# Kernel optimization log

Hardware: AMD Instinct MI355X
Metric: run time of the kernel (lower is better)

## Reference

```python
import jax, jax.numpy as jnp
import numpy as np

# Block(type='a'): dim=256, mlp_ratio=2, qk_dim=64, att_cr=0.5 (pdim=128), sr=2, inp_group=1
DIM, QK, PD, HID, SR = 256, 64, 128, 512, 2
EPS = 1e-5
SCALE = QK ** -0.5


def _conv(x, w, stride=1, pad=0, groups=1):
    return jax.lax.conv_general_dilated(
        x, w, (stride, stride), [(pad, pad), (pad, pad)],
        feature_group_count=groups,
        dimension_numbers=('NCHW', 'OIHW', 'NCHW'))


def _bn(x, s, b):
    # BatchNorm2d in inference/reparam form: per-channel affine
    return x * s[:, None, None] + b[:, None, None]


def setup_inputs() -> dict:
    key = jax.random.key(0)
    ks = jax.random.split(key, 16)
    B, H, W = 16, 64, 64
    x = jax.random.normal(ks[0], (B, DIM, H, W), jnp.float32)
    def w(k, shape):  # conv weights
        return jax.random.normal(k, shape, jnp.float32) * 0.02
    def sb(k, c):     # bn scale / bias
        k1, k2 = jax.random.split(k)
        return (1.0 + 0.1 * jax.random.normal(k1, (c,), jnp.float32),
                0.1 * jax.random.normal(k2, (c,), jnp.float32))
    s_in, b_in = sb(ks[2], 2 * QK + DIM)
    s_k, b_k = sb(ks[4], QK)
    s_v, b_v = sb(ks[6], PD)
    s_out, b_out = sb(ks[8], DIM)
    s1, b1 = sb(ks[10], HID)
    s2, b2 = sb(ks[12], DIM)
    return dict(
        x=x,
        gn_w=1.0 + 0.1 * jax.random.normal(ks[13], (DIM,), jnp.float32),
        gn_b=0.1 * jax.random.normal(ks[14], (DIM,), jnp.float32),
        w_in=w(ks[1], (2 * QK + DIM, DIM, 3, 3)), s_in=s_in, b_in=b_in,
        w_k=w(ks[3], (QK, 1, SR, SR)), s_k=s_k, b_k=b_k,
        w_v=w(ks[5], (PD, 1, SR, SR)), s_v=s_v, b_v=b_v,
        w_out=w(ks[7], (DIM, DIM, 1, 1)), s_out=s_out, b_out=b_out,
        w1=w(ks[9], (HID, DIM, 1, 1)), s1=s1, b1=b1,
        w2=w(ks[11], (DIM, HID, 1, 1)), s2=s2, b2=b2,
    )


def reference(x, gn_w, gn_b, w_in, s_in, b_in, w_k, s_k, b_k, w_v, s_v, b_v,
              w_out, s_out, b_out, w1, s1, b1, w2, s2, b2):
    B, _, H, W = x.shape
    # --- LRSHA branch ---
    # GroupNorm(1, dim): normalize over (C,H,W) per sample, per-channel affine
    mu = jnp.mean(x, axis=(1, 2, 3), keepdims=True)
    var = jnp.var(x, axis=(1, 2, 3), keepdims=True)
    xn = (x - mu) * jax.lax.rsqrt(var + EPS)
    xn = xn * gn_w[:, None, None] + gn_b[:, None, None]
    t = _bn(_conv(xn, w_in, stride=1, pad=1), s_in, b_in)  # [B, 2*QK+DIM, H, W]
    q, k, v, u = jnp.split(t, [QK, 2 * QK, 2 * QK + PD], axis=1)
    k = _bn(_conv(k, w_k, stride=SR, groups=QK), s_k, b_k)  # [B,QK,H/2,W/2]
    v = _bn(_conv(v, w_v, stride=SR, groups=PD), s_v, b_v)  # [B,PD,H/2,W/2]
    qf = q.reshape(B, QK, H * W)          # [B, QK, N]
    kf = k.reshape(B, QK, -1)             # [B, QK, M]
    vf = v.reshape(B, PD, -1)             # [B, PD, M]
    attn = jax.nn.softmax(jnp.einsum('bcn,bcm->bnm', qf, kf) * SCALE, axis=-1)
    a = jnp.einsum('bpm,bnm->bpn', vf, attn).reshape(B, PD, H, W)
    cat = jnp.concatenate([a, u], axis=1)  # [B, DIM, H, W]
    att_out = _bn(_conv(jax.nn.relu(cat), w_out), s_out, b_out)
    x1 = x + att_out  # residual
    # --- FFN branch (1x1 conv -> ReLU -> 1x1 conv) ---
    h = jax.nn.relu(_bn(_conv(x1, w1), s1, b1))
    ffn = _bn(_conv(h, w2), s2, b2)
    return x1 + ffn
```

## Files before the change

### kernel.cpp

```cpp
#include <hip/hip_runtime.h>
#include <hip/hip_bf16.h>

#define DIM 256
#define QK 64
#define PD 128
#define HID 512
#define NPX 4096
#define NB 16
#define SCALE 0.125f
#define GN_EPS 1e-5f

typedef short bf16x8 __attribute__((ext_vector_type(8)));
typedef float f32x4 __attribute__((ext_vector_type(4)));
#define MFMA16(a, b, c) __builtin_amdgcn_mfma_f32_16x16x32_bf16(a, b, c, 0, 0, 0)

__device__ __forceinline__ unsigned f2b(float f) {
    unsigned u = __float_as_uint(f);
    return (u + 0x7fffu + ((u >> 16) & 1u)) >> 16;
}
__device__ __forceinline__ float b2f(unsigned short s) {
    return __uint_as_float((unsigned)s << 16);
}

__global__ __launch_bounds__(256) void gn_part_kernel(const float* __restrict__ x, float* __restrict__ part) {
    int chunk = blockIdx.x, b = blockIdx.y;
    const float* xp = x + (size_t)b * (DIM * NPX) + (size_t)chunk * 16384;
    float s = 0.f, ss = 0.f;
    for (int i = threadIdx.x; i < 16384; i += 256) { float v = xp[i]; s += v; ss += v * v; }
    for (int off = 32; off > 0; off >>= 1) { s += __shfl_down(s, off); ss += __shfl_down(ss, off); }
    __shared__ float red[8];
    int w = threadIdx.x >> 6;
    if ((threadIdx.x & 63) == 0) { red[w * 2] = s; red[w * 2 + 1] = ss; }
    __syncthreads();
    if (threadIdx.x == 0) {
        float S = red[0] + red[2] + red[4] + red[6];
        float SS = red[1] + red[3] + red[5] + red[7];
        part[(b * 64 + chunk) * 2] = S;
        part[(b * 64 + chunk) * 2 + 1] = SS;
    }
}

__global__ __launch_bounds__(256) void gn_final_kernel(const float* __restrict__ part,
                                                       const float* __restrict__ gn_w, const float* __restrict__ gn_b,
                                                       float* __restrict__ Aarr, float* __restrict__ Barr) {
    int b = blockIdx.x;
    float s = 0.f, ss = 0.f;
    if (threadIdx.x < 64) {
        s = part[(b * 64 + threadIdx.x) * 2];
        ss = part[(b * 64 + threadIdx.x) * 2 + 1];
        for (int off = 32; off > 0; off >>= 1) { s += __shfl_down(s, off); ss += __shfl_down(ss, off); }
    }
    __shared__ float sh[2];
    if (threadIdx.x == 0) {
        const float invN = 1.f / (float)(DIM * NPX);
        float mu = s * invN;
        float var = ss * invN - mu * mu;
        sh[0] = mu; sh[1] = rsqrtf(var + GN_EPS);
    }
    __syncthreads();
    float mu = sh[0], rstd = sh[1];
    int c = threadIdx.x;
    float g = gn_w[c] * rstd;
    Aarr[b * 256 + c] = g;
    Barr[b * 256 + c] = gn_b[c] - mu * g;
}

__global__ __launch_bounds__(256) void xnb_kernel(const float* __restrict__ x,
                                                  const float* __restrict__ Aarr, const float* __restrict__ Barr,
                                                  unsigned short* __restrict__ xb) {
    int y = blockIdx.x, b = blockIdx.y;
    int tid = threadIdx.x;
    __shared__ unsigned short tile[64 * 264];
    const float* xr = x + ((size_t)b << 20) + (size_t)y * 64;
    const float* Ab = Aarr + b * 256;
    const float* Bb = Barr + b * 256;
    for (int it = 0; it < 64; it++) {
        int lin = it * 256 + tid;
        int c = lin >> 6, px = lin & 63;
        float v = fmaf(xr[((size_t)c << 12) + px], Ab[c], Bb[c]);
        tile[px * 264 + c] = (unsigned short)f2b(v);
    }
    __syncthreads();
    unsigned short* ob = xb + (((size_t)(b * 64 + y)) << 14);
    for (int it = 0; it < 8; it++) {
        int lin = it * 256 + tid;
        int px = lin >> 5, g = lin & 31;
        *(uint4*)&ob[px * 256 + g * 8] = *(const uint4*)&tile[px * 264 + g * 8];
    }
}

__global__ __launch_bounds__(256) void wcvt_kernel(const float* __restrict__ w_in, const float* __restrict__ w_out,
                                                   const float* __restrict__ w1, const float* __restrict__ w2,
                                                   unsigned short* __restrict__ wb2, unsigned short* __restrict__ wob,
                                                   unsigned short* __restrict__ w1b, unsigned short* __restrict__ w2b) {
    int idx = blockIdx.x * 256 + threadIdx.x;
    if (idx < 884736) {
        int ci = idx & 31;
        int oc = (idx >> 5) % 384;
        int tapck = idx / 12288;
        int ck = tapck / 9, tap = tapck % 9;
        wb2[idx] = (unsigned short)f2b(w_in[((size_t)oc * 256 + ck * 32 + ci) * 9 + tap]);
    } else if (idx < 950272) {
        int j = idx - 884736;
        wob[j] = (unsigned short)f2b(w_out[j]);
    } else if (idx < 1081344) {
        int j = idx - 950272;
        w1b[j] = (unsigned short)f2b(w1[j]);
    } else if (idx < 1212416) {
        int j = idx - 1081344;
        w2b[j] = (unsigned short)f2b(w2[j]);
    }
}

__global__ __launch_bounds__(256, 3) void conv3_mfma_kernel(const unsigned short* __restrict__ xb,
                                                            const unsigned short* __restrict__ wb2,
                                                            const float* __restrict__ s_in, const float* __restrict__ b_in,
                                                            unsigned short* __restrict__ tcl) {
    int wgid = blockIdx.x;
    int tile = (wgid & 7) * 96 + (wgid >> 3);
    int ocb = tile % 6;
    int tmp = tile / 6;
    int rg2 = tmp & 7, b = tmp >> 3;
    int tid = threadIdx.x;
    int w = tid >> 6, lane = tid & 63, g = lane >> 4, l15 = lane & 15;
    __shared__ unsigned short xs[6 * 66 * 40];
    int oc0 = ocb * 64;
    if (tid < 48) {
        int row = tid >> 3, cp = (tid >> 2) & 1, gg = tid & 3;
        int col = cp ? 65 : 0;
        *(uint4*)&xs[(row * 66 + col) * 40 + gg * 8] = make_uint4(0, 0, 0, 0);
    }
    const unsigned short* xg = xb + ((size_t)b << 20);
    for (int half = 0; half < 2; half++) {
        int y0 = rg2 * 8 + half * 4;
        f32x4 acc[4][4];
#pragma unroll
        for (int o = 0; o < 4; o++)
#pragma unroll
            for (int p = 0; p < 4; p++)
#pragma unroll
                for (int r = 0; r < 4; r++) acc[o][p][r] = 0.f;
        for (int ck = 0; ck < 8; ck++) {
            int ci0 = ck * 32;
            __syncthreads();
#pragma unroll
            for (int it = 0; it < 6; it++) {
                int lin = it * 256 + tid;
                int gg = lin & 3, col = (lin >> 2) & 63, row = lin >> 8;
                int y = y0 - 1 + row;
                uint4 val = make_uint4(0, 0, 0, 0);
                if (y >= 0 && y < 64)
                    val = *(const uint4*)(xg + (((size_t)(y * 64 + col)) << 8) + ci0 + gg * 8);
                *(uint4*)&xs[(row * 66 + col + 1) * 40 + gg * 8] = val;
            }
            __syncthreads();
            const unsigned short* wp = wb2 + (size_t)ck * 9 * 384 * 32;
#pragma unroll
            for (int tap = 0; tap < 9; tap++) {
                int dy = tap / 3, dx = tap % 3;
                bf16x8 Af[4], Bf[4];
#pragma unroll
                for (int o = 0; o < 4; o++)
                    Af[o] = *(const bf16x8*)(wp + ((size_t)tap * 384 + oc0 + o * 16 + l15) * 32 + g * 8);
#pragma unroll
                for (int p = 0; p < 4; p++)
                    Bf[p] = *(const bf16x8*)&xs[((w + dy) * 66 + p * 16 + l15 + dx) * 40 + g * 8];
#pragma unroll
                for (int o = 0; o < 4; o++)
#pragma unroll
                    for (int p = 0; p < 4; p++)
                        acc[o][p] = MFMA16(Af[o], Bf[p], acc[o][p]);
            }
        }
        int y = y0 + w;
        unsigned short* tout = tcl + ((size_t)(b * 4096 + y * 64)) * 384;
#pragma unroll
        for (int o = 0; o < 4; o++) {
            int ocb4 = oc0 + o * 16 + 4 * g;
            float s0 = s_in[ocb4], s1 = s_in[ocb4 + 1], s2 = s_in[ocb4 + 2], s3 = s_in[ocb4 + 3];
            float b0 = b_in[ocb4], b1 = b_in[ocb4 + 1], b2 = b_in[ocb4 + 2], b3 = b_in[ocb4 + 3];
#pragma unroll
            for (int p = 0; p < 4; p++) {
                ushort4 h;
                h.x = (unsigned short)f2b(fmaf(acc[o][p][0], s0, b0));
                h.y = (unsigned short)f2b(fmaf(acc[o][p][1], s1, b1));
                h.z = (unsigned short)f2b(fmaf(acc[o][p][2], s2, b2));
                h.w = (unsigned short)f2b(fmaf(acc[o][p][3], s3, b3));
                *(ushort4*)&tout[(size_t)(p * 16 + l15) * 384 + ocb4] = h;
            }
        }
    }
}

__global__ __launch_bounds__(256) void dw_kernel(const unsigned short* __restrict__ tcl,
                                                 const float* __restrict__ w_k, const float* __restrict__ s_k, const float* __restrict__ b_k,
                                                 const float* __restrict__ w_v, const float* __restrict__ s_v, const float* __restrict__ b_v,
                                                 unsigned short* __restrict__ kd_t, unsigned short* __restrict__ vd_b) {
    int mg = blockIdx.x, b = blockIdx.y;
    int m0 = mg * 64;
    int tid = threadIdx.x;
    __shared__ unsigned short vt[128 * 68];
    {
        int c = tid & 63;
        float4 wk4 = *(const float4*)(w_k + c * 4);
        float sc = s_k[c], bi = b_k[c];
#pragma unroll 4
        for (int it = 0; it < 16; it++) {
            int ml = it * 4 + (tid >> 6);
            int m = m0 + ml, yo = m >> 5, xo = m & 31;
            const unsigned short* s = tcl + ((size_t)(b * 4096 + yo * 128 + xo * 2)) * 384 + 64 + c;
            float v = wk4.x * b2f(s[0]) + wk4.y * b2f(s[384]) + wk4.z * b2f(s[24576]) + wk4.w * b2f(s[24960]);
            kd_t[((size_t)(b * 1024 + m) << 6) + c] = (unsigned short)f2b(fmaf(v, sc, bi));
        }
    }
    {
        int c2 = tid & 127;
        float4 wv4 = *(const float4*)(w_v + c2 * 4);
        float sc = s_v[c2], bi = b_v[c2];
#pragma unroll 4
        for (int it = 0; it < 32; it++) {
            int ml = it * 2 + (tid >> 7);
            int m = m0 + ml, yo = m >> 5, xo = m & 31;
            const unsigned short* s = tcl + ((size_t)(b * 4096 + yo * 128 + xo * 2)) * 384 + 128 + c2;
            float v = wv4.x * b2f(s[0]) + wv4.y * b2f(s[384]) + wv4.z * b2f(s[24576]) + wv4.w * b2f(s[24960]);
            vt[c2 * 68 + ml] = (unsigned short)f2b(fmaf(v, sc, bi));
        }
    }
    __syncthreads();
    {
        int c2 = tid >> 1, part = tid & 1;
        unsigned short* dst = vd_b + (((size_t)(b * 128 + c2)) << 10) + m0 + part * 32;
        const unsigned short* src = &vt[c2 * 68 + part * 32];
#pragma unroll
        for (int j = 0; j < 8; j++)
            *(ushort4*)(dst + j * 4) = *(const ushort4*)(src + j * 4);
    }
}

__global__ __launch_bounds__(256) void attn_mfma_kernel(const unsigned short* __restrict__ tcl,
                                                        const unsigned short* __restrict__ kd_t,
                                                        const unsigned short* __restrict__ vd_b,
                                                        unsigned short* __restrict__ apx) {
    int tid = threadIdx.x;
    int wid = tid >> 6, lane = tid & 63;
    int g = lane >> 4, l15 = lane & 15;
    int b = blockIdx.y;
    int n0 = (blockIdx.x * 4 + wid) * 32;

    __shared__ char KsB[8192];
    __shared__ char VsB[16384];
    __shared__ unsigned short ot[4][32][136];

    bf16x8 qf[2][2];
#pragma unroll
    for (int nf = 0; nf < 2; nf++)
#pragma unroll
        for (int kc = 0; kc < 2; kc++)
            qf[nf][kc] = *(const bf16x8*)(tcl + ((size_t)(b * 4096 + n0 + 16 * nf + l15)) * 384 + kc * 32 + g * 8);

    f32x4 O[8][2];
#pragma unroll
    for (int pt = 0; pt < 8; pt++)
#pragma unroll
        for (int nf = 0; nf < 2; nf++)
#pragma unroll
            for (int r = 0; r < 4; r++) O[pt][nf][r] = 0.f;
    float mr[2] = {-1e30f, -1e30f}, lr[2] = {0.f, 0.f};

    const unsigned short* kb = kd_t + ((size_t)b << 16);
    const unsigned short* vb = vd_b + ((size_t)(b * 128) << 10);

    union BU { unsigned u[4]; bf16x8 v; };
    int srcA = l15 + ((g & 1) << 5);
    int srcB = srcA + 16;
    bool hi = (g >> 1) != 0;
    int srow = tid >> 3, sch = tid & 7;

    for (int mt = 0; mt < 16; mt++) {
        int m0 = mt * 64;
        __syncthreads();
#pragma unroll
        for (int it = 0; it < 2; it++) {
            int row = it * 32 + srow;
            uint4 v = *(const uint4*)(kb + (((size_t)(m0 + row)) << 6) + sch * 8);
            *(uint4*)(KsB + row * 128 + ((sch * 16) ^ ((row & 7) << 4))) = v;
        }
#pragma unroll
        for (int it = 0; it < 4; it++) {
            int row = it * 32 + srow;
            uint4 v = *(const uint4*)(vb + (((size_t)row) << 10) + m0 + sch * 8);
            *(uint4*)(VsB + row * 128 + ((sch * 16) ^ ((row & 7) << 4))) = v;
        }
        __syncthreads();
        f32x4 sp[4][2];
#pragma unroll
        for (int f = 0; f < 4; f++)
#pragma unroll
            for (int nf = 0; nf < 2; nf++)
#pragma unroll
                for (int r = 0; r < 4; r++) sp[f][nf][r] = 0.f;
#pragma unroll
        for (int f = 0; f < 4; f++) {
#pragma unroll
            for (int kc = 0; kc < 2; kc++) {
                bf16x8 kf = *(const bf16x8*)(KsB + (16 * f + l15) * 128 + ((kc * 64 + g * 16) ^ ((l15 & 7) << 4)));
                sp[f][0] = MFMA16(kf, qf[0][kc], sp[f][0]);
                sp[f][1] = MFMA16(kf, qf[1][kc], sp[f][1]);
            }
        }
        BU Bp[2][2];
#pragma unroll
        for (int nf = 0; nf < 2; nf++) {
            float tmax = -1e30f;
#pragma unroll
            for (int f = 0; f < 4; f++)
#pragma unroll
                for (int r = 0; r < 4; r++) tmax = fmaxf(tmax, sp[f][nf][r]);
            tmax = fmaxf(tmax, __shfl_xor(tmax, 16));
            tmax = fmaxf(tmax, __shfl_xor(tmax, 32));
            float newm = fmaxf(mr[nf], tmax * SCALE);
            float fac = __expf(mr[nf] - newm);
            float ps = 0.f;
            unsigned pl[4], ph[4];
#pragma unroll
            for (int f = 0; f < 4; f++) {
                float p0 = __expf(fmaf(sp[f][nf][0], SCALE, -newm));
                float p1 = __expf(fmaf(sp[f][nf][1], SCALE, -newm));
                float p2 = __expf(fmaf(sp[f][nf][2], SCALE, -newm));
                float p3 = __expf(fmaf(sp[f][nf][3], SCALE, -newm));
                ps += (p0 + p1) + (p2 + p3);
                pl[f] = f2b(p0) | (f2b(p1) << 16);
                ph[f] = f2b(p2) | (f2b(p3) << 16);
            }
            ps += __shfl_xor(ps, 16);
            ps += __shfl_xor(ps, 32);
            lr[nf] = fmaf(lr[nf], fac, ps);
            mr[nf] = newm;
#pragma unroll
            for (int pt = 0; pt < 8; pt++)
#pragma unroll
                for (int r = 0; r < 4; r++) O[pt][nf][r] *= fac;
#pragma unroll
            for (int kc = 0; kc < 2; kc++) {
                unsigned a0 = (unsigned)__shfl((int)pl[2 * kc], srcA);
                unsigned a1 = (unsigned)__shfl((int)ph[2 * kc], srcA);
                unsigned b0 = (unsigned)__shfl((int)pl[2 * kc + 1], srcA);
                unsigned b1 = (unsigned)__shfl((int)ph[2 * kc + 1], srcA);
                unsigned a2 = (unsigned)__shfl((int)pl[2 * kc], srcB);
                unsigned a3 = (unsigned)__shfl((int)ph[2 * kc], srcB);
                unsigned b2 = (unsigned)__shfl((int)pl[2 * kc + 1], srcB);
                unsigned b3 = (unsigned)__shfl((int)ph[2 * kc + 1], srcB);
                Bp[nf][kc].u[0] = hi ? b0 : a0;
                Bp[nf][kc].u[1] = hi ? b1 : a1;
                Bp[nf][kc].u[2] = hi ? b2 : a2;
                Bp[nf][kc].u[3] = hi ? b3 : a3;
            }
        }
#pragma unroll
        for (int pt = 0; pt < 8; pt++) {
            int p = pt * 16 + l15;
#pragma unroll
            for (int kc = 0; kc < 2; kc++) {
                bf16x8 vf = *(const bf16x8*)(VsB + p * 128 + ((kc * 64 + g * 16) ^ ((p & 7) << 4)));
                O[pt][0] = MFMA16(vf, Bp[0][kc].v, O[pt][0]);
                O[pt][1] = MFMA16(vf, Bp[1][kc].v, O[pt][1]);
            }
        }
    }
    float inv0 = 1.f / lr[0], inv1 = 1.f / lr[1];
#pragma unroll
    for (int pt = 0; pt < 8; pt++) {
#pragma unroll
        for (int r = 0; r < 4; r++) {
            int prow = pt * 16 + 4 * g + r;
            ot[wid][l15][prow]      = (unsigned short)f2b(fmaxf(O[pt][0][r] * inv0, 0.f));
            ot[wid][l15 + 16][prow] = (unsigned short)f2b(fmaxf(O[pt][1][r] * inv1, 0.f));
        }
    }
#pragma unroll
    for (int j = 0; j < 8; j++) {
        int lin = j * 64 + lane;
        int row = lin >> 4, cg = lin & 15;
        *(uint4*)&apx[((size_t)(b * 4096 + n0 + row)) * 128 + cg * 8] = *(const uint4*)&ot[wid][row][cg * 8];
    }
}

__global__ __launch_bounds__(256) void catconv_mfma_kernel(const unsigned short* __restrict__ apx,
                                                           const unsigned short* __restrict__ tcl,
                                                           const unsigned short* __restrict__ wob,
                                                           const float* __restrict__ x,
                                                           const float* __restrict__ s_out, const float* __restrict__ b_out,
                                                           float* __restrict__ out, unsigned short* __restrict__ x1cl) {
    int tid = threadIdx.x;
    int w = tid >> 6, lane = tid & 63, g = lane >> 4, l15 = lane & 15;
    int b = blockIdx.z;
    int px0 = blockIdx.x * 256 + w * 64;
    int co0 = blockIdx.y * 64;
    f32x4 acc[4][4];
#pragma unroll
    for (int o = 0; o < 4; o++)
#pragma unroll
        for (int p = 0; p < 4; p++)
#pragma unroll
            for (int r = 0; r < 4; r++) acc[o][p][r] = 0.f;
    const unsigned short* ab = apx + (((size_t)b * 4096) << 7);
    const unsigned short* ub = tcl + ((size_t)b * 4096) * 384 + 256;
    for (int kc = 0; kc < 8; kc++) {
        bf16x8 Af[4], Bf[4];
#pragma unroll
        for (int o = 0; o < 4; o++)
            Af[o] = *(const bf16x8*)(wob + (size_t)(co0 + o * 16 + l15) * 256 + kc * 32 + g * 8);
        if (kc < 4) {
#pragma unroll
            for (int p = 0; p < 4; p++)
                Bf[p] = *(const bf16x8*)(ab + ((size_t)(px0 + p * 16 + l15) << 7) + kc * 32 + g * 8);
        } else {
#pragma unroll
            for (int p = 0; p < 4; p++) {
                bf16x8 v = *(const bf16x8*)(ub + (size_t)(px0 + p * 16 + l15) * 384 + (kc - 4) * 32 + g * 8);
#pragma unroll
                for (int j = 0; j < 8; j++) {
                    unsigned short s = (unsigned short)v[j];
                    v[j] = (short)((s & 0x8000u) ? 0 : s);
                }
                Bf[p] = v;
            }
        }
#pragma unroll
        for (int o = 0; o < 4; o++)
#pragma unroll
            for (int p = 0; p < 4; p++)
                acc[o][p] = MFMA16(Af[o], Bf[p], acc[o][p]);
    }
#pragma unroll
    for (int o = 0; o < 4; o++) {
        int co_b = co0 + o * 16 + 4 * g;
#pragma unroll
        for (int r = 0; r < 4; r++) {
            int co = co_b + r;
            float sc = s_out[co], bi = b_out[co];
            size_t base = (((size_t)b * 256 + co) << 12) + px0 + l15;
#pragma unroll
            for (int p = 0; p < 4; p++) {
                float res = x[base + p * 16] + fmaf(acc[o][p][r], sc, bi);
                out[base + p * 16] = res;
                acc[o][p][r] = res;
            }
        }
#pragma unroll
        for (int p = 0; p < 4; p++) {
            ushort4 h;
            h.x = (unsigned short)f2b(acc[o][p][0]);
            h.y = (unsigned short)f2b(acc[o][p][1]);
            h.z = (unsigned short)f2b(acc[o][p][2]);
            h.w = (unsigned short)f2b(acc[o][p][3]);
            *(ushort4*)&x1cl[((size_t)(b * 4096 + px0 + p * 16 + l15)) * 256 + co_b] = h;
        }
    }
}

__global__ __launch_bounds__(256) void ffn1_mfma_kernel(const unsigned short* __restrict__ x1cl,
                                                        const unsigned short* __restrict__ w1b,
                                                        const float* __restrict__ s1, const float* __restrict__ b1,
                                                        unsigned short* __restrict__ hcl) {
    int tid = threadIdx.x;
    int w = tid >> 6, lane = tid & 63, g = lane >> 4, l15 = lane & 15;
    int b = blockIdx.z;
    int px0 = blockIdx.x * 256 + w * 64;
    int hc0 = blockIdx.y * 64;
    f32x4 acc[4][4];
#pragma unroll
    for (int p = 0; p < 4; p++)
#pragma unroll
        for (int o = 0; o < 4; o++)
#pragma unroll
            for (int r = 0; r < 4; r++) acc[p][o][r] = 0.f;
    const unsigned short* xb = x1cl + (((size_t)b * 4096) << 8);
    for (int kc = 0; kc < 8; kc++) {
        bf16x8 Af[4], Bf[4];
#pragma unroll
        for (int p = 0; p < 4; p++)
            Af[p] = *(const bf16x8*)(xb + ((size_t)(px0 + p * 16 + l15) << 8) + kc * 32 + g * 8);
#pragma unroll
        for (int o = 0; o < 4; o++)
            Bf[o] = *(const bf16x8*)(w1b + (size_t)(hc0 + o * 16 + l15) * 256 + kc * 32 + g * 8);
#pragma unroll
        for (int p = 0; p < 4; p++)
#pragma unroll
            for (int o = 0; o < 4; o++)
                acc[p][o] = MFMA16(Af[p], Bf[o], acc[p][o]);
    }
    unsigned short* hb = hcl + (((size_t)b * 4096) << 9);
#pragma unroll
    for (int o = 0; o < 4; o++) {
        int hc = hc0 + o * 16 + l15;
        float sc = s1[hc], bi = b1[hc];
#pragma unroll
        for (int p = 0; p < 4; p++) {
#pragma unroll
            for (int r = 0; r < 4; r++) {
                int px = px0 + p * 16 + 4 * g + r;
                hb[((size_t)px << 9) + hc] = (unsigned short)f2b(fmaxf(fmaf(acc[p][o][r], sc, bi), 0.f));
            }
        }
    }
}

__global__ __launch_bounds__(256) void ffn2_mfma_kernel(const unsigned short* __restrict__ hcl,
                                                        const unsigned short* __restrict__ w2b,
                                                        const float* __restrict__ s2, const float* __restrict__ b2,
                                                        float* __restrict__ out) {
    int tid = threadIdx.x;
    int w = tid >> 6, lane = tid & 63, g = lane >> 4, l15 = lane & 15;
    int b = blockIdx.z;
    int px0 = blockIdx.x * 256 + w * 64;
    int co0 = blockIdx.y * 64;
    f32x4 acc[4][4];
#pragma unroll
    for (int o = 0; o < 4; o++)
#pragma unroll
        for (int p = 0; p < 4; p++)
#pragma unroll
            for (int r = 0; r < 4; r++) acc[o][p][r] = 0.f;
    const unsigned short* hb = hcl + (((size_t)b * 4096) << 9);
    for (int kc = 0; kc < 16; kc++) {
        bf16x8 Af[4], Bf[4];
#pragma unroll
        for (int o = 0; o < 4; o++)
            Af[o] = *(const bf16x8*)(w2b + (size_t)(co0 + o * 16 + l15) * 512 + kc * 32 + g * 8);
#pragma unroll
        for (int p = 0; p < 4; p++)
            Bf[p] = *(const bf16x8*)(hb + ((size_t)(px0 + p * 16 + l15) << 9) + kc * 32 + g * 8);
#pragma unroll
        for (int o = 0; o < 4; o++)
#pragma unroll
            for (int p = 0; p < 4; p++)
                acc[o][p] = MFMA16(Af[o], Bf[p], acc[o][p]);
    }
#pragma unroll
    for (int o = 0; o < 4; o++) {
#pragma unroll
        for (int r = 0; r < 4; r++) {
            int co = co0 + o * 16 + 4 * g + r;
            float sc = s2[co], bi = b2[co];
            size_t base = (((size_t)b * 256 + co) << 12) + px0 + l15;
#pragma unroll
            for (int p = 0; p < 4; p++)
                out[base + p * 16] = out[base + p * 16] + fmaf(acc[o][p][r], sc, bi);
        }
    }
}

extern "C" void kernel_launch(void* const* d_in, const int* in_sizes, int n_in,
                              void* d_out, int out_size, void* d_ws, size_t ws_size,
                              hipStream_t stream) {
    const float* x    = (const float*)d_in[0];
    const float* gn_w = (const float*)d_in[1];
    const float* gn_b = (const float*)d_in[2];
    const float* w_in = (const float*)d_in[3];
    const float* s_in = (const float*)d_in[4];
    const float* b_in = (const float*)d_in[5];
    const float* w_k  = (const float*)d_in[6];
    const float* s_k  = (const float*)d_in[7];
    const float* b_k  = (const float*)d_in[8];
    const float* w_v  = (const float*)d_in[9];
    const float* s_v  = (const float*)d_in[10];
    const float* b_v  = (const float*)d_in[11];
    const float* w_out= (const float*)d_in[12];
    const float* s_out= (const float*)d_in[13];
    const float* b_out= (const float*)d_in[14];
    const float* w1   = (const float*)d_in[15];
    const float* s1   = (const float*)d_in[16];
    const float* b1   = (const float*)d_in[17];
    const float* w2   = (const float*)d_in[18];
    const float* s2   = (const float*)d_in[19];
    const float* b2   = (const float*)d_in[20];
    float* out = (float*)d_out;
    float* ws = (float*)d_ws;

    float* part = ws;
    float* Aarr = ws + 2048;
    float* Barr = ws + 6144;
    unsigned short* tcl = (unsigned short*)(ws + 10240);
    unsigned short* xb   = (unsigned short*)(ws + 12593152);
    unsigned short* x1cl = (unsigned short*)(ws + 12593152);
    unsigned short* apx  = (unsigned short*)(ws + 20981760);
    unsigned short* hcl  = (unsigned short*)(ws + 20981760);
    unsigned short* kd_t = (unsigned short*)(ws + 37758976);
    unsigned short* vd_b = (unsigned short*)(ws + 38283264);
    unsigned short* wb2  = (unsigned short*)(ws + 39331840);
    unsigned short* wob  = (unsigned short*)(ws + 39774208);
    unsigned short* w1b  = (unsigned short*)(ws + 39806976);
    unsigned short* w2b  = (unsigned short*)(ws + 39872512);

    gn_part_kernel<<<dim3(64, 16), 256, 0, stream>>>(x, part);
    gn_final_kernel<<<16, 256, 0, stream>>>(part, gn_w, gn_b, Aarr, Barr);
    xnb_kernel<<<dim3(64, 16), 256, 0, stream>>>(x, Aarr, Barr, xb);
    wcvt_kernel<<<4736, 256, 0, stream>>>(w_in, w_out, w1, w2, wb2, wob, w1b, w2b);
    conv3_mfma_kernel<<<768, 256, 0, stream>>>(xb, wb2, s_in, b_in, tcl);
    dw_kernel<<<dim3(16, 16), 256, 0, stream>>>(tcl, w_k, s_k, b_k, w_v, s_v, b_v, kd_t, vd_b);
    attn_mfma_kernel<<<dim3(32, 16), 256, 0, stream>>>(tcl, kd_t, vd_b, apx);
    catconv_mfma_kernel<<<dim3(16, 4, 16), 256, 0, stream>>>(apx, tcl, wob, x, s_out, b_out, out, x1cl);
    ffn1_mfma_kernel<<<dim3(16, 8, 16), 256, 0, stream>>>(x1cl, w1b, s1, b1, hcl);
    ffn2_mfma_kernel<<<dim3(16, 4, 16), 256, 0, stream>>>(hcl, w2b, s2, b2, out);
}
```

Measured before the change: 516.2 us.

## Double attention KV tile size, use exp2 softmax with lazy rescaling

Raises the key/value tile in the flash-attention kernel from 64 to 128 positions, which halves the loop trips and the barrier pairs. Softmax moves to exp2 with a folded log2e scale. The running max and the O rescale are now updated only when the new max exceeds the old one by a threshold, so most tiles skip the rescale multiplies. The output staging buffer now reuses the K/V shared memory after a barrier, which offsets part of the larger LDS footprint, but register pressure rises from the doubled score tile.

```diff
diff --git a/kernel.cpp b/kernel.cpp
--- a/kernel.cpp
+++ b/kernel.cpp
@@ -247,9 +247,11 @@
     int b = blockIdx.y;
     int n0 = (blockIdx.x * 4 + wid) * 32;
 
-    __shared__ char KsB[8192];
-    __shared__ char VsB[16384];
-    __shared__ unsigned short ot[4][32][136];
+    __shared__ char smem[49152];
+    char* KsB = smem;
+    char* VsB = smem + 16384;
+
+    const float SC2 = 0.18033688011112042f;
 
     bf16x8 qf[2][2];
 #pragma unroll
@@ -274,33 +276,34 @@
     int srcA = l15 + ((g & 1) << 5);
     int srcB = srcA + 16;
     bool hi = (g >> 1) != 0;
-    int srow = tid >> 3, sch = tid & 7;
-
-    for (int mt = 0; mt < 16; mt++) {
-        int m0 = mt * 64;
+    int srow8 = tid >> 3, sch8 = tid & 7;
+    int srow16 = tid >> 4, sch16 = tid & 15;
+
+    for (int mt = 0; mt < 8; mt++) {
+        int m0 = mt * 128;
         __syncthreads();
 #pragma unroll
-        for (int it = 0; it < 2; it++) {
-            int row = it * 32 + srow;
-            uint4 v = *(const uint4*)(kb + (((size_t)(m0 + row)) << 6) + sch * 8);
-            *(uint4*)(KsB + row * 128 + ((sch * 16) ^ ((row & 7) << 4))) = v;
-        }
-#pragma unroll
         for (int it = 0; it < 4; it++) {
-            int row = it * 32 + srow;
-            uint4 v = *(const uint4*)(vb + (((size_t)row) << 10) + m0 + sch * 8);
-            *(uint4*)(VsB + row * 128 + ((sch * 16) ^ ((row & 7) << 4))) = v;
+            int row = it * 32 + srow8;
+            uint4 v = *(const uint4*)(kb + (((size_t)(m0 + row)) << 6) + sch8 * 8);
+            *(uint4*)(KsB + row * 128 + ((sch8 * 16) ^ ((row & 7) << 4))) = v;
+        }
+#pragma unroll
+        for (int it = 0; it < 8; it++) {
+            int row = it * 16 + srow16;
+            uint4 v = *(const uint4*)(vb + (((size_t)row) << 10) + m0 + sch16 * 8);
+            *(uint4*)(VsB + row * 256 + ((sch16 * 16) ^ ((row & 15) << 4))) = v;
         }
         __syncthreads();
-        f32x4 sp[4][2];
-#pragma unroll
-        for (int f = 0; f < 4; f++)
+        f32x4 sp[8][2];
+#pragma unroll
+        for (int f = 0; f < 8; f++)
 #pragma unroll
             for (int nf = 0; nf < 2; nf++)
 #pragma unroll
                 for (int r = 0; r < 4; r++) sp[f][nf][r] = 0.f;
 #pragma unroll
-        for (int f = 0; f < 4; f++) {
+        for (int f = 0; f < 8; f++) {
 #pragma unroll
             for (int kc = 0; kc < 2; kc++) {
                 bf16x8 kf = *(const bf16x8*)(KsB + (16 * f + l15) * 128 + ((kc * 64 + g * 16) ^ ((l15 & 7) << 4)));
@@ -308,40 +311,44 @@
                 sp[f][1] = MFMA16(kf, qf[1][kc], sp[f][1]);
             }
         }
-        BU Bp[2][2];
+        BU Bp[2][4];
 #pragma unroll
         for (int nf = 0; nf < 2; nf++) {
             float tmax = -1e30f;
 #pragma unroll
-            for (int f = 0; f < 4; f++)
+            for (int f = 0; f < 8; f++)
 #pragma unroll
                 for (int r = 0; r < 4; r++) tmax = fmaxf(tmax, sp[f][nf][r]);
             tmax = fmaxf(tmax, __shfl_xor(tmax, 16));
             tmax = fmaxf(tmax, __shfl_xor(tmax, 32));
-            float newm = fmaxf(mr[nf], tmax * SCALE);
-            float fac = __expf(mr[nf] - newm);
+            float tm2 = tmax * SC2;
+            if (!__all(tm2 <= mr[nf] + 11.0f)) {
+                float newm = fmaxf(mr[nf], tm2);
+                float fac = exp2f(mr[nf] - newm);
+                lr[nf] *= fac;
+#pragma unroll
+                for (int pt = 0; pt < 8; pt++)
+#pragma unroll
+                    for (int r = 0; r < 4; r++) O[pt][nf][r] *= fac;
+                mr[nf] = newm;
+            }
             float ps = 0.f;
-            unsigned pl[4], ph[4];
-#pragma unroll
-            for (int f = 0; f < 4; f++) {
-                float p0 = __expf(fmaf(sp[f][nf][0], SCALE, -newm));
-                float p1 = __expf(fmaf(sp[f][nf][1], SCALE, -newm));
-                float p2 = __expf(fmaf(sp[f][nf][2], SCALE, -newm));
-                float p3 = __expf(fmaf(sp[f][nf][3], SCALE, -newm));
+            unsigned pl[8], ph[8];
+#pragma unroll
+            for (int f = 0; f < 8; f++) {
+                float p0 = exp2f(fmaf(sp[f][nf][0], SC2, -mr[nf]));
+                float p1 = exp2f(fmaf(sp[f][nf][1], SC2, -mr[nf]));
+                float p2 = exp2f(fmaf(sp[f][nf][2], SC2, -mr[nf]));
+                float p3 = exp2f(fmaf(sp[f][nf][3], SC2, -mr[nf]));
                 ps += (p0 + p1) + (p2 + p3);
                 pl[f] = f2b(p0) | (f2b(p1) << 16);
                 ph[f] = f2b(p2) | (f2b(p3) << 16);
             }
             ps += __shfl_xor(ps, 16);
             ps += __shfl_xor(ps, 32);
-            lr[nf] = fmaf(lr[nf], fac, ps);
-            mr[nf] = newm;
-#pragma unroll
-            for (int pt = 0; pt < 8; pt++)
-#pragma unroll
-                for (int r = 0; r < 4; r++) O[pt][nf][r] *= fac;
-#pragma unroll
-            for (int kc = 0; kc < 2; kc++) {
+            lr[nf] += ps;
+#pragma unroll
+            for (int kc = 0; kc < 4; kc++) {
                 unsigned a0 = (unsigned)__shfl((int)pl[2 * kc], srcA);
                 unsigned a1 = (unsigned)__shfl((int)ph[2 * kc], srcA);
                 unsigned b0 = (unsigned)__shfl((int)pl[2 * kc + 1], srcA);
@@ -360,13 +367,15 @@
         for (int pt = 0; pt < 8; pt++) {
             int p = pt * 16 + l15;
 #pragma unroll
-            for (int kc = 0; kc < 2; kc++) {
-                bf16x8 vf = *(const bf16x8*)(VsB + p * 128 + ((kc * 64 + g * 16) ^ ((p & 7) << 4)));
+            for (int kc = 0; kc < 4; kc++) {
+                bf16x8 vf = *(const bf16x8*)(VsB + p * 256 + ((kc * 64 + g * 16) ^ ((p & 15) << 4)));
                 O[pt][0] = MFMA16(vf, Bp[0][kc].v, O[pt][0]);
                 O[pt][1] = MFMA16(vf, Bp[1][kc].v, O[pt][1]);
             }
         }
     }
+    __syncthreads();
+    unsigned short (*ot)[32][136] = (unsigned short (*)[32][136])smem;
     float inv0 = 1.f / lr[0], inv1 = 1.f / lr[1];
 #pragma unroll
     for (int pt = 0; pt < 8; pt++) {
```

New measurement: 519.2 us. Within noise of the previous version (+0.6%).
